# Kernel optimization log

Measured on AMD Instinct MI355X. Metric: run time of the kernel, lower is better.

The kernel has to match this reference:

```python
import jax, jax.numpy as jnp
import numpy as np

N = 100000   # nodes per node type
E = 300000   # edges per relation
HID = 128
HEADS = 2
C = HID // HEADS  # 64 per-head channels
IN = 16
NEG_SLOPE = 0.2


def _gatv2(x_src, x_dst, ei, Wl, Wr, att, b):
    """PyG GATv2Conv, add_self_loops=False, share_weights=False, concat heads."""
    n_dst = x_dst.shape[0]
    src, dst = ei[0], ei[1]
    gl = (x_src @ Wl).reshape(-1, HEADS, C)[src]   # [E,H,C] gathered source messages
    gr = (x_dst @ Wr).reshape(-1, HEADS, C)[dst]   # [E,H,C]
    e = jnp.einsum('ehc,hc->eh', jax.nn.leaky_relu(gl + gr, NEG_SLOPE), att)  # [E,H]
    emax = jax.ops.segment_max(e, dst, num_segments=n_dst)       # per-dst max (softmax stability)
    p = jnp.exp(e - emax[dst])
    denom = jax.ops.segment_sum(p, dst, num_segments=n_dst)
    alpha = p / (denom[dst] + 1e-16)                              # scatter-softmax
    out = jax.ops.segment_sum(alpha[..., None] * gl, dst, num_segments=n_dst)
    return out.reshape(n_dst, HEADS * C) + b


def _hetero_layer(ht, hv, he, eis, Wl, Wr, att, bc):
    # relation order: 0 t->t, 1 t->v, 2 v->t, 3 t->e, 4 e->t, 5 v->e, 6 e->v, 7 v->v, 8 e->e
    g = lambda i, xs, xd: _gatv2(xs, xd, eis[i], Wl[i], Wr[i], att[i], bc[i])
    ot = g(0, ht, ht) + g(2, hv, ht) + g(4, he, ht)   # aggr='sum' over dst=tile
    ov = g(1, ht, hv) + g(6, he, hv) + g(7, hv, hv)   # dst=vertex
    oe = g(3, ht, he) + g(5, hv, he) + g(8, he, he)   # dst=edge
    return ot, ov, oe


def setup_inputs() -> dict:
    key = jax.random.key(0)
    ks = jax.random.split(key, 32)
    d = {
        'xt': jax.random.normal(ks[0], (N, IN), jnp.float32),
        'xv': jax.random.normal(ks[1], (N, IN), jnp.float32),
        'xe': jax.random.normal(ks[2], (N, IN), jnp.float32),
    }
    names = ['ei_tt', 'ei_tv', 'ei_vt', 'ei_te', 'ei_et', 'ei_ve', 'ei_ev', 'ei_vv', 'ei_ee']
    for i, nm in enumerate(names):
        d[nm] = jax.random.randint(ks[3 + i], (2, E), 0, N, dtype=jnp.int32)
    s_in = 1.0 / np.sqrt(IN)
    s_h = 1.0 / np.sqrt(HID)
    for j, t in enumerate(['t', 'v', 'e']):
        d[f'W{t}'] = jax.random.uniform(ks[12 + j], (IN, HID), jnp.float32, -s_in, s_in)
        d[f'b{t}'] = jax.random.uniform(ks[15 + j], (HID,), jnp.float32, -s_in, s_in)
    for l in (1, 2):
        o = 18 + (l - 1) * 4
        d[f'Wl{l}'] = jax.random.uniform(ks[o], (9, HID, HID), jnp.float32, -s_h, s_h)
        d[f'Wr{l}'] = jax.random.uniform(ks[o + 1], (9, HID, HID), jnp.float32, -s_h, s_h)
        d[f'att{l}'] = jax.random.uniform(ks[o + 2], (9, HEADS, C), jnp.float32, -s_h, s_h)
        d[f'bc{l}'] = jnp.zeros((9, HID), jnp.float32)
    return d


def reference(xt, xv, xe, ei_tt, ei_tv, ei_vt, ei_te, ei_et, ei_ve, ei_ev, ei_vv, ei_ee,
              Wt, bt, Wv, bv, We, be, Wl1, Wr1, att1, bc1, Wl2, Wr2, att2, bc2):
    eis = [ei_tt, ei_tv, ei_vt, ei_te, ei_et, ei_ve, ei_ev, ei_vv, ei_ee]
    ht = xt @ Wt + bt  # in_proj per node type
    hv = xv @ Wv + bv
    he = xe @ We + be
    ht, hv, he = _hetero_layer(ht, hv, he, eis, Wl1, Wr1, att1, bc1)
    ht, hv, he = jax.nn.relu(ht), jax.nn.relu(hv), jax.nn.relu(he)
    ht, hv, he = _hetero_layer(ht, hv, he, eis, Wl2, Wr2, att2, bc2)
    return jnp.concatenate([ht, hv, he], axis=0)  # [3N, HID]
```

## Files before the change

### kernel.cpp

```cpp
#include <hip/hip_runtime.h>


#define NN 100000
#define NE 300000
#define NH (NN * 128)
#define NB 391
#define LOG2E 1.4426950408889634f

typedef __attribute__((ext_vector_type(8))) short short8;
typedef __attribute__((ext_vector_type(4))) float f32x4;

__device__ __forceinline__ float bf2f(unsigned short h) {
    return __uint_as_float(((unsigned)h) << 16);
}
__device__ __forceinline__ unsigned short f2bf(float x) {
    unsigned u = __float_as_uint(x);
    return (unsigned short)((u + 0x7FFFu + ((u >> 16) & 1u)) >> 16);
}

struct EPtrs { const int* p[9]; };
struct G6 { const unsigned short* A[6]; const float* W[6]; unsigned short* O[6]; };
struct GatA {
    const unsigned short* PL[3];
    const unsigned short* PR[3];
    const int* rowp[3];
    const int* csrc[3];
    const float* att[3];
    const float* bias[3];
};

__global__ void inproj_k(const float* __restrict__ X, const float* __restrict__ W,
                         const float* __restrict__ b, unsigned short* __restrict__ H, int M) {
    int w = (int)((blockIdx.x * blockDim.x + threadIdx.x) >> 6);
    int lane = threadIdx.x & 63;
    if (w >= M) return;
    const float* x = X + (long)w * 16;
    float a0 = 0.f, a1 = 0.f;
#pragma unroll
    for (int k = 0; k < 16; ++k) {
        float xv = x[k];
        a0 = fmaf(xv, W[k * 128 + lane], a0);
        a1 = fmaf(xv, W[k * 128 + 64 + lane], a1);
    }
    H[(long)w * 128 + lane] = f2bf(a0 + b[lane]);
    H[(long)w * 128 + 64 + lane] = f2bf(a1 + b[64 + lane]);
}

__global__ __launch_bounds__(256) void gemm6_k(G6 g, int M) {
    __shared__ unsigned short Bt[128 * 136];
    int which = blockIdx.y;
    const unsigned short* A = g.A[which];
    const float* W = g.W[which];
    unsigned short* O = g.O[which];
    int tid = threadIdx.x;
#pragma unroll
    for (int i = 0; i < 64; ++i) {
        int idx = i * 256 + tid;
        int k = idx >> 7, c = idx & 127;
        Bt[c * 136 + k] = f2bf(W[idx]);
    }
    __syncthreads();
    int wv = tid >> 6, lane = tid & 63;
    int quad = lane >> 4, l15 = lane & 15;
    long rowbase = (long)blockIdx.x * 64 + wv * 16;
    long arow = rowbase + l15;
    if (arow > M - 1) arow = M - 1;
    f32x4 acc[8];
#pragma unroll
    for (int n = 0; n < 8; ++n) acc[n] = (f32x4){0.f, 0.f, 0.f, 0.f};
#pragma unroll
    for (int kb = 0; kb < 4; ++kb) {
        short8 a = *(const short8*)(A + arow * 128 + kb * 32 + quad * 8);
#pragma unroll
        for (int n = 0; n < 8; ++n) {
            short8 b = *(const short8*)(&Bt[(n * 16 + l15) * 136 + kb * 32 + quad * 8]);
            acc[n] = __builtin_amdgcn_mfma_f32_16x16x32_bf16(a, b, acc[n], 0, 0, 0);
        }
    }
#pragma unroll
    for (int n = 0; n < 8; ++n)
#pragma unroll
        for (int r = 0; r < 4; ++r) {
            long row = rowbase + quad * 4 + r;
            if (row < M) O[row * 128 + n * 16 + l15] = f2bf(acc[n][r]);
        }
}

__global__ void count_k(EPtrs ep, int* __restrict__ deg) {
    int r = blockIdx.y;
    int e = blockIdx.x * 256 + threadIdx.x;
    if (e >= NE) return;
    atomicAdd(&deg[r * NN + ep.p[r][NE + e]], 1);
}

__global__ void scanA_k(const int* __restrict__ deg, int* __restrict__ bsum) {
    __shared__ int sm[256];
    int r = blockIdx.y, b = blockIdx.x, t = threadIdx.x;
    int i = b * 256 + t;
    sm[t] = (i < NN) ? deg[r * NN + i] : 0;
    __syncthreads();
#pragma unroll
    for (int o = 128; o; o >>= 1) {
        if (t < o) sm[t] += sm[t + o];
        __syncthreads();
    }
    if (t == 0) bsum[r * NB + b] = sm[0];
}

__global__ void scanB_k(int* __restrict__ bsum) {
    __shared__ int sm[512];
    int r = blockIdx.x, t = threadIdx.x;
    int v = (t < NB) ? bsum[r * NB + t] : 0;
    sm[t] = v;
    __syncthreads();
    for (int o = 1; o < 512; o <<= 1) {
        int x = (t >= o) ? sm[t - o] : 0;
        __syncthreads();
        sm[t] += x;
        __syncthreads();
    }
    if (t < NB) bsum[r * NB + t] = sm[t] - v;
}

__global__ void scanC_k(int* __restrict__ deg, const int* __restrict__ bsum,
                        int* __restrict__ rowp) {
    __shared__ int sm[256];
    int r = blockIdx.y, b = blockIdx.x, t = threadIdx.x;
    int i = b * 256 + t;
    int v = (i < NN) ? deg[r * NN + i] : 0;
    sm[t] = v;
    __syncthreads();
    for (int o = 1; o < 256; o <<= 1) {
        int x = (t >= o) ? sm[t - o] : 0;
        __syncthreads();
        sm[t] += x;
        __syncthreads();
    }
    int excl = sm[t] - v + bsum[r * NB + b];
    if (i < NN) {
        rowp[r * (NN + 1) + i] = excl;
        deg[r * NN + i] = excl;
        if (i == NN - 1) rowp[r * (NN + 1) + NN] = excl + v;
    }
}

__global__ void scat_k(EPtrs ep, int* __restrict__ cursor, int* __restrict__ csrc) {
    int r = blockIdx.y;
    int e = blockIdx.x * 256 + threadIdx.x;
    if (e >= NE) return;
    int s = ep.p[r][e], d = ep.p[r][NE + e];
    int pos = atomicAdd(&cursor[r * NN + d], 1);
    csrc[(long)r * NE + pos] = s;
}

__global__ void gat3_k(GatA g, float* __restrict__ outF, unsigned short* __restrict__ outH,
                       int mode) {
    int w = (int)((blockIdx.x * blockDim.x + threadIdx.x) >> 6);
    int l = threadIdx.x & 63;
    if (w >= NN) return;
    int col = ((l >> 5) << 6) + ((l & 31) << 1);

    const unsigned short* PL0 = g.PL[0];
    const unsigned short* PL1 = g.PL[1];
    const unsigned short* PL2 = g.PL[2];
    const int* cs0 = g.csrc[0];
    const int* cs1 = g.csrc[1];
    const int* cs2 = g.csrc[2];

    unsigned grp0 = *(const unsigned*)(g.PR[0] + (long)w * 128 + col);
    unsigned grp1 = *(const unsigned*)(g.PR[1] + (long)w * 128 + col);
    unsigned grp2 = *(const unsigned*)(g.PR[2] + (long)w * 128 + col);
    float gr00 = __uint_as_float(grp0 << 16), gr01 = __uint_as_float(grp0 & 0xffff0000u);
    float gr10 = __uint_as_float(grp1 << 16), gr11 = __uint_as_float(grp1 & 0xffff0000u);
    float gr20 = __uint_as_float(grp2 << 16), gr21 = __uint_as_float(grp2 & 0xffff0000u);
    float at00 = g.att[0][col] * LOG2E, at01 = g.att[0][col + 1] * LOG2E;
    float at10 = g.att[1][col] * LOG2E, at11 = g.att[1][col + 1] * LOG2E;
    float at20 = g.att[2][col] * LOG2E, at21 = g.att[2][col + 1] * LOG2E;

    int i0 = g.rowp[0][w], e0 = g.rowp[0][w + 1];
    int i1 = g.rowp[1][w], e1 = g.rowp[1][w + 1];
    int i2 = g.rowp[2][w], e2 = g.rowp[2][w + 1];

    float m0 = -1e30f, sd0 = 0.f, A00 = 0.f, A01 = 0.f;
    float m1 = -1e30f, sd1 = 0.f, A10 = 0.f, A11 = 0.f;
    float m2 = -1e30f, sd2 = 0.f, A20 = 0.f, A21 = 0.f;

    bool h0 = i0 < e0, h1 = i1 < e1, h2 = i2 < e2;
    unsigned nx0 = 0, nx1 = 0, nx2 = 0;
    if (h0) {
        int s = __builtin_amdgcn_readfirstlane(cs0[i0]);
        nx0 = *(const unsigned*)(PL0 + (long)s * 128 + col);
    }
    if (h1) {
        int s = __builtin_amdgcn_readfirstlane(cs1[i1]);
        nx1 = *(const unsigned*)(PL1 + (long)s * 128 + col);
    }
    if (h2) {
        int s = __builtin_amdgcn_readfirstlane(cs2[i2]);
        nx2 = *(const unsigned*)(PL2 + (long)s * 128 + col);
    }

#define GSTEP(gg, gr_0, gr_1, at_0, at_1, m_, sd_, A_0, A_1)                  \
    {                                                                         \
        float gl0 = __uint_as_float((gg) << 16);                              \
        float gl1 = __uint_as_float((gg) & 0xffff0000u);                      \
        float x0 = gl0 + (gr_0), x1 = gl1 + (gr_1);                           \
        float t0 = fmaxf(x0, 0.f) + 0.2f * fminf(x0, 0.f);                    \
        float t1 = fmaxf(x1, 0.f) + 0.2f * fminf(x1, 0.f);                    \
        float v = t0 * (at_0) + t1 * (at_1);                                  \
        v += __shfl_xor(v, 16);                                               \
        v += __shfl_xor(v, 8);                                                \
        v += __shfl_xor(v, 4);                                                \
        v += __shfl_xor(v, 2);                                                \
        v += __shfl_xor(v, 1);                                                \
        float mn = fmaxf(m_, v);                                              \
        float sc = __builtin_exp2f(m_ - mn);                                  \
        float p = __builtin_exp2f(v - mn);                                    \
        sd_ = sd_ * sc + p;                                                   \
        A_0 = A_0 * sc + p * gl0;                                             \
        A_1 = A_1 * sc + p * gl1;                                             \
        m_ = mn;                                                              \
    }

    while (h0 || h1 || h2) {
        if (h0) {
            unsigned gg = nx0;
            ++i0;
            h0 = i0 < e0;
            if (h0) {
                int s = __builtin_amdgcn_readfirstlane(cs0[i0]);
                nx0 = *(const unsigned*)(PL0 + (long)s * 128 + col);
            }
            GSTEP(gg, gr00, gr01, at00, at01, m0, sd0, A00, A01);
        }
        if (h1) {
            unsigned gg = nx1;
            ++i1;
            h1 = i1 < e1;
            if (h1) {
                int s = __builtin_amdgcn_readfirstlane(cs1[i1]);
                nx1 = *(const unsigned*)(PL1 + (long)s * 128 + col);
            }
            GSTEP(gg, gr10, gr11, at10, at11, m1, sd1, A10, A11);
        }
        if (h2) {
            unsigned gg = nx2;
            ++i2;
            h2 = i2 < e2;
            if (h2) {
                int s = __builtin_amdgcn_readfirstlane(cs2[i2]);
                nx2 = *(const unsigned*)(PL2 + (long)s * 128 + col);
            }
            GSTEP(gg, gr20, gr21, at20, at21, m2, sd2, A20, A21);
        }
    }
#undef GSTEP

    float acc0 = A00 / (sd0 + 1e-16f) + g.bias[0][col] + A10 / (sd1 + 1e-16f) +
                 g.bias[1][col] + A20 / (sd2 + 1e-16f) + g.bias[2][col];
    float acc1 = A01 / (sd0 + 1e-16f) + g.bias[0][col + 1] + A11 / (sd1 + 1e-16f) +
                 g.bias[1][col + 1] + A21 / (sd2 + 1e-16f) + g.bias[2][col + 1];

    long o = (long)w * 128 + col;
    if (mode == 0) {
        unsigned px = (unsigned)f2bf(fmaxf(acc0, 0.f)) |
                      ((unsigned)f2bf(fmaxf(acc1, 0.f)) << 16);
        *(unsigned*)(outH + o) = px;
    } else {
        *(float2*)(outF + o) = make_float2(acc0, acc1);
    }
}

__global__ void sentinel_k(float* out) { out[0] = 123456.0f; }

extern "C" void kernel_launch(void* const* d_in, const int* in_sizes, int n_in,
                              void* d_out, int out_size, void* d_ws, size_t ws_size,
                              hipStream_t stream) {
    const float* xin[3] = {(const float*)d_in[0], (const float*)d_in[1], (const float*)d_in[2]};
    EPtrs ep;
    for (int r = 0; r < 9; ++r) ep.p[r] = (const int*)d_in[3 + r];
    const float* Win[3] = {(const float*)d_in[12], (const float*)d_in[14], (const float*)d_in[16]};
    const float* bin[3] = {(const float*)d_in[13], (const float*)d_in[15], (const float*)d_in[17]};
    const float* Wl[2] = {(const float*)d_in[18], (const float*)d_in[22]};
    const float* Wr[2] = {(const float*)d_in[19], (const float*)d_in[23]};
    const float* att[2] = {(const float*)d_in[20], (const float*)d_in[24]};
    const float* bc[2] = {(const float*)d_in[21], (const float*)d_in[25]};

    size_t nInt = (size_t)9 * NN + (size_t)9 * NB + (size_t)9 * (NN + 1) + (size_t)9 * NE;
    size_t need = (size_t)12 * NH * 2 + nInt * 4;
    if (ws_size < need) {
        hipMemsetAsync(d_out, 0, (size_t)out_size * 4, stream);
        sentinel_k<<<1, 1, 0, stream>>>((float*)d_out);
        return;
    }
    unsigned short* h1 = (unsigned short*)d_ws;
    unsigned short* h2 = h1 + (size_t)3 * NH;
    unsigned short* pl = h2 + (size_t)3 * NH;
    unsigned short* pr = pl + (size_t)3 * NH;
    int* deg = (int*)(pr + (size_t)3 * NH);
    int* bsum = deg + (size_t)9 * NN;
    int* rowp = bsum + (size_t)9 * NB;
    int* csrc = rowp + (size_t)9 * (NN + 1);

    static const int ST[9] = {0, 0, 1, 0, 2, 1, 2, 1, 2};
    static const int RT[3][3] = {{0, 2, 4}, {1, 6, 7}, {3, 5, 8}};

    for (int T = 0; T < 3; ++T)
        inproj_k<<<NN / 4, 256, 0, stream>>>(xin[T], Win[T], bin[T], h1 + (size_t)T * NH, NN);

    hipMemsetAsync(deg, 0, (size_t)9 * NN * 4, stream);
    dim3 eg((NE + 255) / 256, 9), ng(NB, 9);
    count_k<<<eg, 256, 0, stream>>>(ep, deg);
    scanA_k<<<ng, 256, 0, stream>>>(deg, bsum);
    scanB_k<<<9, 512, 0, stream>>>(bsum);
    scanC_k<<<ng, 256, 0, stream>>>(deg, bsum, rowp);
    scat_k<<<eg, 256, 0, stream>>>(ep, deg, csrc);

    dim3 gg((NN + 63) / 64, 6);
    for (int l = 0; l < 2; ++l) {
        unsigned short* hc = (l == 0) ? h1 : h2;
        for (int T = 0; T < 3; ++T) {
            G6 g6;
            GatA ga;
            for (int j = 0; j < 3; ++j) {
                int r = RT[T][j];
                g6.A[j] = hc + (size_t)ST[r] * NH;
                g6.W[j] = Wl[l] + (size_t)r * 16384;
                g6.O[j] = pl + (size_t)j * NH;
                g6.A[3 + j] = hc + (size_t)T * NH;
                g6.W[3 + j] = Wr[l] + (size_t)r * 16384;
                g6.O[3 + j] = pr + (size_t)j * NH;
                ga.PL[j] = pl + (size_t)j * NH;
                ga.PR[j] = pr + (size_t)j * NH;
                ga.rowp[j] = rowp + (size_t)r * (NN + 1);
                ga.csrc[j] = csrc + (size_t)r * NE;
                ga.att[j] = att[l] + (size_t)r * 128;
                ga.bias[j] = bc[l] + (size_t)r * 128;
            }
            gemm6_k<<<gg, 256, 0, stream>>>(g6, NN);
            if (l == 0)
                gat3_k<<<NN / 4, 256, 0, stream>>>(ga, nullptr, h2 + (size_t)T * NH, 0);
            else
                gat3_k<<<NN / 4, 256, 0, stream>>>(ga, (float*)d_out + (size_t)T * NH, nullptr, 1);
        }
    }
}
```

Baseline: 1.833 ms.

## Pre-transpose weights to bf16 once and prefetch next CSR source index in GAT loop

A new kernel converts all layer weight matrices to transposed bf16 once per call. The GEMM then reads B fragments straight from global memory (likely L2-resident) instead of each block converting and staging the full weight tile in LDS, which removes per-block conversion work and a barrier. Separately, the GAT aggregation loop now loads the source index one edge further ahead, so the dependent index-then-row gather chain is shortened. The tradeoffs are extra global/L2 traffic for B loads in the GEMM and an added kernel launch.

```diff
diff --git a/kernel.cpp b/kernel.cpp
--- a/kernel.cpp
+++ b/kernel.cpp
@@ -19,7 +19,8 @@
 }
 
 struct EPtrs { const int* p[9]; };
-struct G6 { const unsigned short* A[6]; const float* W[6]; unsigned short* O[6]; };
+struct G6 { const unsigned short* A[6]; const unsigned short* WT[6]; unsigned short* O[6]; };
+struct W4 { const float* in[4]; unsigned short* out[4]; };
 struct GatA {
     const unsigned short* PL[3];
     const unsigned short* PR[3];
@@ -46,20 +47,25 @@
     H[(long)w * 128 + 64 + lane] = f2bf(a1 + b[64 + lane]);
 }
 
+__global__ void wcvt_k(W4 w) {
+    int b = blockIdx.x;
+    int a = b / 9, r = b % 9;
+    const float* in = w.in[a] + (long)r * 16384;
+    unsigned short* out = w.out[a] + (long)r * 16384;
+#pragma unroll 4
+    for (int it = 0; it < 64; ++it) {
+        int idx = it * 256 + threadIdx.x;
+        int k = idx >> 7, n = idx & 127;
+        out[n * 128 + k] = f2bf(in[idx]);
+    }
+}
+
 __global__ __launch_bounds__(256) void gemm6_k(G6 g, int M) {
-    __shared__ unsigned short Bt[128 * 136];
     int which = blockIdx.y;
     const unsigned short* A = g.A[which];
-    const float* W = g.W[which];
+    const unsigned short* WT = g.WT[which];
     unsigned short* O = g.O[which];
     int tid = threadIdx.x;
-#pragma unroll
-    for (int i = 0; i < 64; ++i) {
-        int idx = i * 256 + tid;
-        int k = idx >> 7, c = idx & 127;
-        Bt[c * 136 + k] = f2bf(W[idx]);
-    }
-    __syncthreads();
     int wv = tid >> 6, lane = tid & 63;
     int quad = lane >> 4, l15 = lane & 15;
     long rowbase = (long)blockIdx.x * 64 + wv * 16;
@@ -73,7 +79,7 @@
         short8 a = *(const short8*)(A + arow * 128 + kb * 32 + quad * 8);
 #pragma unroll
         for (int n = 0; n < 8; ++n) {
-            short8 b = *(const short8*)(&Bt[(n * 16 + l15) * 136 + kb * 32 + quad * 8]);
+            short8 b = *(const short8*)(WT + (n * 16 + l15) * 128 + kb * 32 + quad * 8);
             acc[n] = __builtin_amdgcn_mfma_f32_16x16x32_bf16(a, b, acc[n], 0, 0, 0);
         }
     }
@@ -187,17 +193,21 @@
 
     bool h0 = i0 < e0, h1 = i1 < e1, h2 = i2 < e2;
     unsigned nx0 = 0, nx1 = 0, nx2 = 0;
+    int sn0 = 0, sn1 = 0, sn2 = 0;
     if (h0) {
         int s = __builtin_amdgcn_readfirstlane(cs0[i0]);
         nx0 = *(const unsigned*)(PL0 + (long)s * 128 + col);
+        if (i0 + 1 < e0) sn0 = __builtin_amdgcn_readfirstlane(cs0[i0 + 1]);
     }
     if (h1) {
         int s = __builtin_amdgcn_readfirstlane(cs1[i1]);
         nx1 = *(const unsigned*)(PL1 + (long)s * 128 + col);
+        if (i1 + 1 < e1) sn1 = __builtin_amdgcn_readfirstlane(cs1[i1 + 1]);
     }
     if (h2) {
         int s = __builtin_amdgcn_readfirstlane(cs2[i2]);
         nx2 = *(const unsigned*)(PL2 + (long)s * 128 + col);
+        if (i2 + 1 < e2) sn2 = __builtin_amdgcn_readfirstlane(cs2[i2 + 1]);
     }
 
 #define GSTEP(gg, gr_0, gr_1, at_0, at_1, m_, sd_, A_0, A_1)                  \
@@ -225,32 +235,35 @@
     while (h0 || h1 || h2) {
         if (h0) {
             unsigned gg = nx0;
-            ++i0;
-            h0 = i0 < e0;
+            int ip = i0 + 1;
+            h0 = ip < e0;
             if (h0) {
-                int s = __builtin_amdgcn_readfirstlane(cs0[i0]);
-                nx0 = *(const unsigned*)(PL0 + (long)s * 128 + col);
+                nx0 = *(const unsigned*)(PL0 + (long)sn0 * 128 + col);
+                if (ip + 1 < e0) sn0 = __builtin_amdgcn_readfirstlane(cs0[ip + 1]);
             }
+            i0 = ip;
             GSTEP(gg, gr00, gr01, at00, at01, m0, sd0, A00, A01);
         }
         if (h1) {
             unsigned gg = nx1;
-            ++i1;
-            h1 = i1 < e1;
+            int ip = i1 + 1;
+            h1 = ip < e1;
             if (h1) {
-                int s = __builtin_amdgcn_readfirstlane(cs1[i1]);
-                nx1 = *(const unsigned*)(PL1 + (long)s * 128 + col);
+                nx1 = *(const unsigned*)(PL1 + (long)sn1 * 128 + col);
+                if (ip + 1 < e1) sn1 = __builtin_amdgcn_readfirstlane(cs1[ip + 1]);
             }
+            i1 = ip;
             GSTEP(gg, gr10, gr11, at10, at11, m1, sd1, A10, A11);
         }
         if (h2) {
             unsigned gg = nx2;
-            ++i2;
-            h2 = i2 < e2;
+            int ip = i2 + 1;
+            h2 = ip < e2;
             if (h2) {
-                int s = __builtin_amdgcn_readfirstlane(cs2[i2]);
-                nx2 = *(const unsigned*)(PL2 + (long)s * 128 + col);
+                nx2 = *(const unsigned*)(PL2 + (long)sn2 * 128 + col);
+                if (ip + 1 < e2) sn2 = __builtin_amdgcn_readfirstlane(cs2[ip + 1]);
             }
+            i2 = ip;
             GSTEP(gg, gr20, gr21, at20, at21, m2, sd2, A20, A21);
         }
     }
@@ -287,7 +300,7 @@
     const float* bc[2] = {(const float*)d_in[21], (const float*)d_in[25]};
 
     size_t nInt = (size_t)9 * NN + (size_t)9 * NB + (size_t)9 * (NN + 1) + (size_t)9 * NE;
-    size_t need = (size_t)12 * NH * 2 + nInt * 4;
+    size_t need = ((size_t)12 * NH + 589824) * 2 + nInt * 4;
     if (ws_size < need) {
         hipMemsetAsync(d_out, 0, (size_t)out_size * 4, stream);
         sentinel_k<<<1, 1, 0, stream>>>((float*)d_out);
@@ -297,7 +310,8 @@
     unsigned short* h2 = h1 + (size_t)3 * NH;
     unsigned short* pl = h2 + (size_t)3 * NH;
     unsigned short* pr = pl + (size_t)3 * NH;
-    int* deg = (int*)(pr + (size_t)3 * NH);
+    unsigned short* wT = pr + (size_t)3 * NH;
+    int* deg = (int*)(wT + 589824);
     int* bsum = deg + (size_t)9 * NN;
     int* rowp = bsum + (size_t)9 * NB;
     int* csrc = rowp + (size_t)9 * (NN + 1);
@@ -307,6 +321,13 @@
 
     for (int T = 0; T < 3; ++T)
         inproj_k<<<NN / 4, 256, 0, stream>>>(xin[T], Win[T], bin[T], h1 + (size_t)T * NH, NN);
+
+    {
+        W4 w4;
+        w4.in[0] = Wl[0]; w4.in[1] = Wr[0]; w4.in[2] = Wl[1]; w4.in[3] = Wr[1];
+        for (int a = 0; a < 4; ++a) w4.out[a] = wT + (size_t)a * 9 * 16384;
+        wcvt_k<<<36, 256, 0, stream>>>(w4);
+    }
 
     hipMemsetAsync(deg, 0, (size_t)9 * NN * 4, stream);
     dim3 eg((NE + 255) / 256, 9), ng(NB, 9);
@@ -325,10 +346,10 @@
             for (int j = 0; j < 3; ++j) {
                 int r = RT[T][j];
                 g6.A[j] = hc + (size_t)ST[r] * NH;
-                g6.W[j] = Wl[l] + (size_t)r * 16384;
+                g6.WT[j] = wT + (size_t)(l * 2 + 0) * 9 * 16384 + (size_t)r * 16384;
                 g6.O[j] = pl + (size_t)j * NH;
                 g6.A[3 + j] = hc + (size_t)T * NH;
-                g6.W[3 + j] = Wr[l] + (size_t)r * 16384;
+                g6.WT[3 + j] = wT + (size_t)(l * 2 + 1) * 9 * 16384 + (size_t)r * 16384;
                 g6.O[3 + j] = pr + (size_t)j * NH;
                 ga.PL[j] = pl + (size_t)j * NH;
                 ga.PR[j] = pr + (size_t)j * NH;
```

Result: slower. 2.416 ms (+31.8%).
